# Optimization experiments

Hardware: AMD Instinct MI355X
Metric: run time of the kernel (lower is better)

The kernel has to match this reference:

```python
import jax, jax.numpy as jnp
import numpy as np

H = 32   # hidden_dim
L = 2    # rnn_num_layers
T = 52   # num_steps / seq_len
F = 64   # n_features (== 2*H, so layer-1 input size matches layer-0)
B = 8192 # batch


def _cell(x, h, c, Wih, Whh, b):
    # PyTorch LSTM gate order: i, f, g, o. b = b_ih + b_hh (mathematically identical).
    g = x @ Wih.T + h @ Whh.T + b
    i, f, gg, o = jnp.split(g, 4, axis=-1)
    c2 = jax.nn.sigmoid(f) * c + jax.nn.sigmoid(i) * jnp.tanh(gg)
    h2 = jax.nn.sigmoid(o) * jnp.tanh(c2)
    return h2, c2


def _encoder(x, h0, c0, Wih, Whh, b):
    # x: [B,T,F]; h0/c0: [2L,B,H]; PyTorch stacking order: [l0_fwd, l0_bwd, l1_fwd, l1_bwd]
    xs = jnp.swapaxes(x, 0, 1)  # time-major [T,B,F]
    hn, cn = [], []
    for l in range(L):
        def step_fwd(carry, xt):
            h, c = carry
            h2, c2 = _cell(xt, h, c, Wih[l, 0], Whh[l, 0], b[l, 0])
            return (h2, c2), h2
        def step_bwd(carry, xt):
            h, c = carry
            h2, c2 = _cell(xt, h, c, Wih[l, 1], Whh[l, 1], b[l, 1])
            return (h2, c2), h2
        (hf, cf), of = jax.lax.scan(step_fwd, (h0[2 * l], c0[2 * l]), xs)
        (hb, cb), ob = jax.lax.scan(step_bwd, (h0[2 * l + 1], c0[2 * l + 1]), xs[::-1])
        xs = jnp.concatenate([of, ob[::-1]], axis=-1)  # [T,B,2H]
        hn += [hf, hb]
        cn += [cf, cb]
    hn = jnp.stack(hn)  # [4,B,H]
    cn = jnp.stack(cn)
    hc = jnp.concatenate([jnp.swapaxes(hn, 0, 1), jnp.swapaxes(cn, 0, 1)], axis=1)  # [B,8,H]
    return hc.reshape(hc.shape[0], -1)  # [B, 2*2L*H] = [B,256]


def _decoder(code, Wih, Whh, b):
    Bn = code.shape[0]
    _code = code.reshape(Bn, 2, 2 * L, H)       # [B, (h,c), 4, H]
    h = jnp.swapaxes(_code[:, 0], 0, 1)          # [4,B,H]
    c = jnp.swapaxes(_code[:, 1], 0, 1)
    out0 = jnp.zeros((Bn, F), code.dtype)

    def step(carry, _):
        out, h, c = carry
        y = out
        hs, cs = [], []
        for l in range(L):
            hf, cf = _cell(y, h[2 * l], c[2 * l], Wih[l, 0], Whh[l, 0], b[l, 0])
            hb, cb = _cell(y, h[2 * l + 1], c[2 * l + 1], Wih[l, 1], Whh[l, 1], b[l, 1])
            y = jnp.concatenate([hf, hb], axis=-1)  # [B,2H]
            hs += [hf, hb]
            cs += [cf, cb]
        return (jax.lax.stop_gradient(y), jnp.stack(hs), jnp.stack(cs)), y

    _, ys = jax.lax.scan(step, (out0, h, c), None, length=T)  # ys: [T,B,F]
    return jnp.swapaxes(ys, 0, 1)  # [B,T,F]


def setup_inputs() -> dict:
    key = jax.random.key(0)
    ks = jax.random.split(key, 9)
    s = 1.0 / np.sqrt(H)  # PyTorch LSTM init range
    u = lambda k, shape: jax.random.uniform(k, shape, jnp.float32, -s, s)
    return {
        "x": jax.random.normal(ks[0], (B, T, F), jnp.float32),
        "h0": jax.random.normal(ks[1], (2 * L, B, H), jnp.float32),
        "c0": jax.random.normal(ks[2], (2 * L, B, H), jnp.float32),
        "enc_Wih": u(ks[3], (L, 2, 4 * H, F)),
        "enc_Whh": u(ks[4], (L, 2, 4 * H, H)),
        "enc_b": u(ks[5], (L, 2, 4 * H)),
        "dec_Wih": u(ks[6], (L, 2, 4 * H, F)),
        "dec_Whh": u(ks[7], (L, 2, 4 * H, H)),
        "dec_b": u(ks[8], (L, 2, 4 * H)),
    }


def reference(x, h0, c0, enc_Wih, enc_Whh, enc_b, dec_Wih, dec_Whh, dec_b):
    z = _encoder(x, h0, c0, enc_Wih, enc_Whh, enc_b)          # [B,256]
    x_hat = _decoder(z, dec_Wih, dec_Whh, dec_b)              # [B,T,F]
    return (x_hat, z)
```

## Files before the change

### kernel.cpp

```cpp
#include <hip/hip_runtime.h>
#include <cstddef>
#include <cstdint>

#define Tn 52
#define Fn 64
#define Hn 32
#define Bn 8192
#define XHAT_ELEMS (Bn * Tn * Fn)
#define L2E 1.44269504088896340736f

typedef __attribute__((ext_vector_type(8))) short bf8v;
typedef __attribute__((ext_vector_type(4))) float f4v;

__device__ __forceinline__ f4v mfma_bf16(bf8v a, bf8v b, f4v c) {
    return __builtin_amdgcn_mfma_f32_16x16x32_bf16(a, b, c, 0, 0, 0);
}

__device__ __forceinline__ unsigned short rne_bf16(float v) {
    unsigned b = __float_as_uint(v);
    unsigned r = ((b >> 16) & 1u) + 0x7FFFu;
    return (unsigned short)((b + r) >> 16);
}

__device__ __forceinline__ bf8v rne8(float4 a, float4 b) {
    float v[8] = {a.x, a.y, a.z, a.w, b.x, b.y, b.z, b.w};
    bf8v r;
#pragma unroll
    for (int j = 0; j < 8; ++j) r[j] = (short)rne_bf16(v[j]);
    return r;
}

__device__ __forceinline__ void lds_barrier() {
    __builtin_amdgcn_sched_barrier(0);
    asm volatile("s_waitcnt lgkmcnt(0)" ::: "memory");
    __builtin_amdgcn_s_barrier();
    __builtin_amdgcn_sched_barrier(0);
}

__device__ __forceinline__ float lstm_one(float aI, float aF, float aG, float aO, float& cst) {
    float ei = exp2f(fminf(40.f, -aI));
    float ef = exp2f(fminf(40.f, -aF));
    float eg = exp2f(fminf(40.f, -aG));
    float eo = exp2f(fminf(40.f, -aO));
    float p   = (1.f + ei) * (1.f + eg);
    float num = cst * p + (1.f - eg) * (1.f + ef);
    float den = (1.f + ef) * p;
    float c2  = num * __builtin_amdgcn_rcpf(den);
    cst = c2;
    float e2 = exp2f(fminf(40.f, -2.f * L2E * c2));
    return (1.f - e2) * __builtin_amdgcn_rcpf((1.f + eo) * (1.f + e2));
}

#define PINW(W)                                                               \
    asm volatile("" : "+v"(W[0][0]), "+v"(W[0][1]), "+v"(W[0][2]),            \
                      "+v"(W[1][0]), "+v"(W[1][1]), "+v"(W[1][2]));           \
    asm volatile("" : "+v"(W[2][0]), "+v"(W[2][1]), "+v"(W[2][2]),            \
                      "+v"(W[3][0]), "+v"(W[3][1]), "+v"(W[3][2]));

__global__ void prep_kernel(const float* __restrict__ eWih, const float* __restrict__ eWhh,
                            const float* __restrict__ dWih, const float* __restrict__ dWhh,
                            unsigned short* __restrict__ ws)
{
    int fid = blockIdx.x * 256 + threadIdx.x;
    if (fid >= 12288) return;
    int lane = fid & 63;
    int ki   = (fid >> 6) % 3;
    int nt   = (fid / 192) & 7;
    int cell = (fid / 1536) & 3;
    int grp  = fid / 6144;
    const float* Wih = grp ? dWih : eWih;
    const float* Whh = grp ? dWhh : eWhh;
    int gate = nt * 16 + (lane & 15);
    float scale = ((gate >> 5) == 2) ? 2.f * L2E : L2E;
    int k0 = ki * 32 + (lane >> 4) * 8;
    size_t base = (size_t)grp * 98304 + (size_t)cell * 12288 + nt * 1536 + ki * 512 + lane * 8;
#pragma unroll
    for (int j = 0; j < 8; ++j) {
        int k = k0 + j;
        float v = (k < 64) ? Wih[(size_t)cell * 8192 + gate * 64 + k]
                           : Whh[(size_t)cell * 4096 + gate * 32 + (k - 64)];
        ws[base + j] = rne_bf16(v * scale);
    }
}

template<int IS_L0>
__global__ __launch_bounds__(256, 2)
void enc_kernel(const float* __restrict__ X, const unsigned short* __restrict__ Xh,
                const float* __restrict__ h0, const float* __restrict__ c0,
                const unsigned short* __restrict__ Whi, const float* __restrict__ bias,
                int layer, unsigned short* __restrict__ outh, float* __restrict__ z)
{
    __shared__ __align__(16) unsigned short Hsh[2][2][16][40];
    const int tid = threadIdx.x, w = tid >> 6, lane = tid & 63;
    const int d = w >> 1, q = w & 1;
    const int a = lane & 15, kb = lane >> 4;
    const int u = q * 16 + a;
    const int row0 = blockIdx.x * 16;
    const int ci = 2 * layer + d;

    bf8v WH[4][3];
#pragma unroll
    for (int g = 0; g < 4; ++g)
#pragma unroll
        for (int ki = 0; ki < 3; ++ki)
            WH[g][ki] = *(const bf8v*)(Whi + (size_t)ci * 12288 + (2 * g + q) * 1536
                                       + ki * 512 + lane * 8);
    float bj[4];
#pragma unroll
    for (int g = 0; g < 4; ++g)
        bj[g] = bias[ci * 128 + g * 32 + u] * ((g == 2) ? 2.f * L2E : L2E);
    float cst[4], hfin[4];
#pragma unroll
    for (int j = 0; j < 4; ++j)
        cst[j] = c0[((size_t)ci * Bn + row0 + 4 * kb + j) * Hn + u];

    {
        int dd = tid >> 7, rr = (tid >> 3) & 15, u4 = (tid & 7) * 4;
        const float* src = h0 + ((size_t)(2 * layer + dd) * Bn + row0 + rr) * Hn + u4;
#pragma unroll
        for (int e = 0; e < 4; ++e)
            Hsh[dd][1][rr][u4 + e] = rne_bf16(src[e]);
    }
    __syncthreads();

    const int grow = row0 + a;
    float4 p0, p1, p2, p3; bf8v ph0, ph1;
    f4v acc[4];
    {
        int tt = d ? (Tn - 1) : 0;
        bf8v xf0, xf1;
        if (IS_L0) {
            const float* sp = X + ((size_t)grow * Tn + tt) * Fn;
            xf0 = rne8(*(const float4*)(sp + kb * 8), *(const float4*)(sp + kb * 8 + 4));
            xf1 = rne8(*(const float4*)(sp + 32 + kb * 8), *(const float4*)(sp + 32 + kb * 8 + 4));
        } else {
            size_t so = ((size_t)tt * Bn + grow) * Fn + kb * 8;
            xf0 = *(const bf8v*)(Xh + so);
            xf1 = *(const bf8v*)(Xh + so + 32);
        }
#pragma unroll
        for (int g = 0; g < 4; ++g) {
            acc[g] = (f4v){bj[g], bj[g], bj[g], bj[g]};
            acc[g] = mfma_bf16(xf0, WH[g][0], acc[g]);
            acc[g] = mfma_bf16(xf1, WH[g][1], acc[g]);
        }
        int tt1 = d ? (Tn - 2) : 1;
        if (IS_L0) {
            const float* sp = X + ((size_t)grow * Tn + tt1) * Fn;
            p0 = *(const float4*)(sp + kb * 8);      p1 = *(const float4*)(sp + kb * 8 + 4);
            p2 = *(const float4*)(sp + 32 + kb * 8); p3 = *(const float4*)(sp + 32 + kb * 8 + 4);
        } else {
            size_t so = ((size_t)tt1 * Bn + grow) * Fn + kb * 8;
            ph0 = *(const bf8v*)(Xh + so);
            ph1 = *(const bf8v*)(Xh + so + 32);
        }
    }

    for (int t = 0; t < Tn; ++t) {
        PINW(WH);
        bf8v hh = *(const bf8v*)&Hsh[d][(t & 1) ^ 1][a][kb * 8];
#pragma unroll
        for (int g = 0; g < 4; ++g) acc[g] = mfma_bf16(hh, WH[g][2], acc[g]);
        int tp = d ? (Tn - 1 - t) : t;
#pragma unroll
        for (int j = 0; j < 4; ++j) {
            float hv = lstm_one(acc[0][j], acc[1][j], acc[2][j], acc[3][j], cst[j]);
            hfin[j] = hv;
            unsigned short hp = rne_bf16(hv);
            Hsh[d][t & 1][4 * kb + j][u] = hp;
            if (IS_L0)
                outh[((size_t)tp * Bn + row0 + 4 * kb + j) * Fn + d * 32 + u] = hp;
        }
        {
            bf8v xf0, xf1;
            if (IS_L0) { xf0 = rne8(p0, p1); xf1 = rne8(p2, p3); }
            else       { xf0 = ph0; xf1 = ph1; }
#pragma unroll
            for (int g = 0; g < 4; ++g) {
                f4v t0 = (f4v){bj[g], bj[g], bj[g], bj[g]};
                t0 = mfma_bf16(xf0, WH[g][0], t0);
                acc[g] = mfma_bf16(xf1, WH[g][1], t0);
            }
            int ts = (t + 2 < Tn) ? t + 2 : Tn - 1;
            int tt = d ? (Tn - 1 - ts) : ts;
            if (IS_L0) {
                const float* sp = X + ((size_t)grow * Tn + tt) * Fn;
                p0 = *(const float4*)(sp + kb * 8);      p1 = *(const float4*)(sp + kb * 8 + 4);
                p2 = *(const float4*)(sp + 32 + kb * 8); p3 = *(const float4*)(sp + 32 + kb * 8 + 4);
            } else {
                size_t so = ((size_t)tt * Bn + grow) * Fn + kb * 8;
                ph0 = *(const bf8v*)(Xh + so);
                ph1 = *(const bf8v*)(Xh + so + 32);
            }
        }
        lds_barrier();
    }
#pragma unroll
    for (int j = 0; j < 4; ++j) {
        size_t zr = (size_t)(row0 + 4 * kb + j) * 256;
        z[zr + ci * 32 + u]       = hfin[j];
        z[zr + 128 + ci * 32 + u] = cst[j];
    }
}

__global__ __launch_bounds__(512, 2)
void dec_kernel(const unsigned short* __restrict__ Whi, const float* __restrict__ bias,
                const float* __restrict__ z, float* __restrict__ xhat)
{
    __shared__ __align__(16) unsigned short Ysh[2][2][16][72];
    __shared__ __align__(16) unsigned short Msh[2][16][72];
    __shared__ __align__(16) unsigned short Hsh[4][2][2][16][40];

    const int tid = threadIdx.x, w = tid >> 6, lane = tid & 63;
    const int P = w >> 2, cl = (w >> 1) & 1, q = w & 1;
    const int cell = P * 2 + cl;
    const int a = lane & 15, kb = lane >> 4, u = q * 16 + a;
    const int row0 = blockIdx.x * 32;

    bf8v WH[4][3];
#pragma unroll
    for (int g = 0; g < 4; ++g)
#pragma unroll
        for (int ki = 0; ki < 3; ++ki)
            WH[g][ki] = *(const bf8v*)(Whi + (size_t)cell * 12288 + (2 * g + q) * 1536
                                       + ki * 512 + lane * 8);
    float bj[4];
#pragma unroll
    for (int g = 0; g < 4; ++g)
        bj[g] = bias[cell * 128 + g * 32 + u] * ((g == 2) ? 2.f * L2E : L2E);

    float cst[2][4];
#pragma unroll
    for (int G = 0; G < 2; ++G)
#pragma unroll
        for (int j = 0; j < 4; ++j)
            cst[G][j] = z[(size_t)(row0 + G * 16 + 4 * kb + j) * 256 + 128 + cell * 32 + u];

    {
        int ct = tid >> 7, rem = tid & 127, rr = rem >> 2, u8 = (rem & 3) * 8;
        const float* src = z + (size_t)(row0 + rr) * 256 + ct * 32 + u8;
#pragma unroll
        for (int e = 0; e < 8; ++e)
            Hsh[ct][rr >> 4][1][rr & 15][u8 + e] = rne_bf16(src[e]);
    }
    __syncthreads();

    f4v accp[4];
    auto hpart = [&](int G, int rpar) {
        bf8v hh = *(const bf8v*)&Hsh[cell][G][rpar][a][kb * 8];
#pragma unroll
        for (int g = 0; g < 4; ++g) {
            f4v t0 = (f4v){bj[g], bj[g], bj[g], bj[g]};
            accp[g] = mfma_bf16(hh, WH[g][2], t0);
        }
    };
    auto finish = [&](int G, int t, bool isA, bool hasV) {
        if (hasV) {
            const unsigned short (*Vh)[72] = isA ? Ysh[G][(t - 1) & 1] : Msh[G];
            bf8v vh0 = *(const bf8v*)&Vh[a][kb * 8];
            bf8v vh1 = *(const bf8v*)&Vh[a][32 + kb * 8];
#pragma unroll
            for (int g = 0; g < 4; ++g) {
                accp[g] = mfma_bf16(vh0, WH[g][0], accp[g]);
                accp[g] = mfma_bf16(vh1, WH[g][1], accp[g]);
            }
        }
#pragma unroll
        for (int j = 0; j < 4; ++j) {
            float hv = lstm_one(accp[0][j], accp[1][j], accp[2][j], accp[3][j], cst[G][j]);
            unsigned short hp = rne_bf16(hv);
            int r = 4 * kb + j;
            Hsh[cell][G][t & 1][r][u] = hp;
            if (isA) {
                Msh[G][r][cl * 32 + u] = hp;
            } else {
                Ysh[G][t & 1][r][cl * 32 + u] = hp;
                xhat[((size_t)(row0 + G * 16 + r) * Tn + t) * Fn + cl * 32 + u] = hv;
            }
        }
    };

    hpart(0, 1);
    for (int t = 0; t < Tn; ++t) {
        PINW(WH);
        if (P == 0) { finish(0, t, true, t > 0);       hpart(1, (t - 1) & 1); }
        else        { if (t > 0) finish(1, t - 1, false, true); hpart(0, (t - 1) & 1); }
        lds_barrier();
        if (P == 0) { finish(1, t, true, t > 0);       hpart(0, t & 1); }
        else        { finish(0, t, false, true);       hpart(1, (t & 1) ^ 1); }
        lds_barrier();
    }
    if (P == 1) finish(1, Tn - 1, false, true);
}

extern "C" void kernel_launch(void* const* d_in, const int* in_sizes, int n_in,
                              void* d_out, int out_size, void* d_ws, size_t ws_size,
                              hipStream_t stream) {
    const float* x    = (const float*)d_in[0];
    const float* h0   = (const float*)d_in[1];
    const float* c0   = (const float*)d_in[2];
    const float* eWih = (const float*)d_in[3];
    const float* eWhh = (const float*)d_in[4];
    const float* eb   = (const float*)d_in[5];
    const float* dWih = (const float*)d_in[6];
    const float* dWhh = (const float*)d_in[7];
    const float* db   = (const float*)d_in[8];

    float* out = (float*)d_out;
    unsigned short* xs1h = (unsigned short*)d_out;
    float* zb = out + (size_t)XHAT_ELEMS;
    unsigned short* wsb = (unsigned short*)d_ws;

    hipLaunchKernelGGL(prep_kernel, dim3(48), dim3(256), 0, stream,
                       eWih, eWhh, dWih, dWhh, wsb);
    hipLaunchKernelGGL((enc_kernel<1>), dim3(Bn / 16), dim3(256), 0, stream,
                       x, (const unsigned short*)nullptr,
                       h0, c0, wsb, eb, 0, xs1h, zb);
    hipLaunchKernelGGL((enc_kernel<0>), dim3(Bn / 16), dim3(256), 0, stream,
                       (const float*)nullptr, xs1h,
                       h0, c0, wsb, eb, 1, (unsigned short*)nullptr, zb);
    hipLaunchKernelGGL(dec_kernel, dim3(Bn / 32), dim3(512), 0, stream,
                       wsb + 98304, db, zb, out);
}
```

Before: 267.6 us.

## Split encoder directions across blocks, unroll time loops, add MFMA priority

The encoder now launches one 128-thread block per direction (grid y = 2) instead of one 256-thread block holding both directions, which halves the barrier group size and shrinks shared memory per block. Both encoder and decoder time loops are unrolled by two so the double-buffer parity is a compile-time constant. Bias is pre-broadcast into vector registers and fed straight into the MFMA accumulator. The decoder MFMA sections are raised with s_setprio, and the sched_barrier fences around the LDS barrier are removed so the compiler can reorder across it. The risks are more, smaller blocks competing for CUs, and different instruction scheduling once the fences are gone.

After: 272.9 us. Within noise of the previous version (+2.0%).

```diff
diff --git a/kernel.cpp b/kernel.cpp
--- a/kernel.cpp
+++ b/kernel.cpp
@@ -31,10 +31,8 @@
 }
 
 __device__ __forceinline__ void lds_barrier() {
-    __builtin_amdgcn_sched_barrier(0);
     asm volatile("s_waitcnt lgkmcnt(0)" ::: "memory");
     __builtin_amdgcn_s_barrier();
-    __builtin_amdgcn_sched_barrier(0);
 }
 
 __device__ __forceinline__ float lstm_one(float aI, float aF, float aG, float aO, float& cst) {
@@ -84,18 +82,18 @@
 }
 
 template<int IS_L0>
-__global__ __launch_bounds__(256, 2)
+__global__ __launch_bounds__(128, 2)
 void enc_kernel(const float* __restrict__ X, const unsigned short* __restrict__ Xh,
                 const float* __restrict__ h0, const float* __restrict__ c0,
                 const unsigned short* __restrict__ Whi, const float* __restrict__ bias,
                 int layer, unsigned short* __restrict__ outh, float* __restrict__ z)
 {
-    __shared__ __align__(16) unsigned short Hsh[2][2][16][40];
-    const int tid = threadIdx.x, w = tid >> 6, lane = tid & 63;
-    const int d = w >> 1, q = w & 1;
+    __shared__ __align__(16) unsigned short Hsh[2][16][40];
+    const int tid = threadIdx.x, q = tid >> 6, lane = tid & 63;
     const int a = lane & 15, kb = lane >> 4;
     const int u = q * 16 + a;
     const int row0 = blockIdx.x * 16;
+    const int d = blockIdx.y;
     const int ci = 2 * layer + d;
 
     bf8v WH[4][3];
@@ -105,21 +103,23 @@
         for (int ki = 0; ki < 3; ++ki)
             WH[g][ki] = *(const bf8v*)(Whi + (size_t)ci * 12288 + (2 * g + q) * 1536
                                        + ki * 512 + lane * 8);
-    float bj[4];
-#pragma unroll
-    for (int g = 0; g < 4; ++g)
-        bj[g] = bias[ci * 128 + g * 32 + u] * ((g == 2) ? 2.f * L2E : L2E);
+    f4v bC[4];
+#pragma unroll
+    for (int g = 0; g < 4; ++g) {
+        float bv = bias[ci * 128 + g * 32 + u] * ((g == 2) ? 2.f * L2E : L2E);
+        bC[g] = (f4v){bv, bv, bv, bv};
+    }
     float cst[4], hfin[4];
 #pragma unroll
     for (int j = 0; j < 4; ++j)
         cst[j] = c0[((size_t)ci * Bn + row0 + 4 * kb + j) * Hn + u];
 
     {
-        int dd = tid >> 7, rr = (tid >> 3) & 15, u4 = (tid & 7) * 4;
-        const float* src = h0 + ((size_t)(2 * layer + dd) * Bn + row0 + rr) * Hn + u4;
+        int rr = tid >> 3, u4 = (tid & 7) * 4;
+        const float* src = h0 + ((size_t)ci * Bn + row0 + rr) * Hn + u4;
 #pragma unroll
         for (int e = 0; e < 4; ++e)
-            Hsh[dd][1][rr][u4 + e] = rne_bf16(src[e]);
+            Hsh[1][rr][u4 + e] = rne_bf16(src[e]);
     }
     __syncthreads();
 
@@ -139,11 +139,8 @@
             xf1 = *(const bf8v*)(Xh + so + 32);
         }
 #pragma unroll
-        for (int g = 0; g < 4; ++g) {
-            acc[g] = (f4v){bj[g], bj[g], bj[g], bj[g]};
-            acc[g] = mfma_bf16(xf0, WH[g][0], acc[g]);
-            acc[g] = mfma_bf16(xf1, WH[g][1], acc[g]);
-        }
+        for (int g = 0; g < 4; ++g)
+            acc[g] = mfma_bf16(xf1, WH[g][1], mfma_bf16(xf0, WH[g][0], bC[g]));
         int tt1 = d ? (Tn - 2) : 1;
         if (IS_L0) {
             const float* sp = X + ((size_t)grow * Tn + tt1) * Fn;
@@ -156,9 +153,9 @@
         }
     }
 
-    for (int t = 0; t < Tn; ++t) {
+    auto step = [&](int t, int par) {
         PINW(WH);
-        bf8v hh = *(const bf8v*)&Hsh[d][(t & 1) ^ 1][a][kb * 8];
+        bf8v hh = *(const bf8v*)&Hsh[par ^ 1][a][kb * 8];
 #pragma unroll
         for (int g = 0; g < 4; ++g) acc[g] = mfma_bf16(hh, WH[g][2], acc[g]);
         int tp = d ? (Tn - 1 - t) : t;
@@ -167,33 +164,32 @@
             float hv = lstm_one(acc[0][j], acc[1][j], acc[2][j], acc[3][j], cst[j]);
             hfin[j] = hv;
             unsigned short hp = rne_bf16(hv);
-            Hsh[d][t & 1][4 * kb + j][u] = hp;
+            Hsh[par][4 * kb + j][u] = hp;
             if (IS_L0)
                 outh[((size_t)tp * Bn + row0 + 4 * kb + j) * Fn + d * 32 + u] = hp;
         }
-        {
-            bf8v xf0, xf1;
-            if (IS_L0) { xf0 = rne8(p0, p1); xf1 = rne8(p2, p3); }
-            else       { xf0 = ph0; xf1 = ph1; }
-#pragma unroll
-            for (int g = 0; g < 4; ++g) {
-                f4v t0 = (f4v){bj[g], bj[g], bj[g], bj[g]};
-                t0 = mfma_bf16(xf0, WH[g][0], t0);
-                acc[g] = mfma_bf16(xf1, WH[g][1], t0);
-            }
-            int ts = (t + 2 < Tn) ? t + 2 : Tn - 1;
-            int tt = d ? (Tn - 1 - ts) : ts;
-            if (IS_L0) {
-                const float* sp = X + ((size_t)grow * Tn + tt) * Fn;
-                p0 = *(const float4*)(sp + kb * 8);      p1 = *(const float4*)(sp + kb * 8 + 4);
-                p2 = *(const float4*)(sp + 32 + kb * 8); p3 = *(const float4*)(sp + 32 + kb * 8 + 4);
-            } else {
-                size_t so = ((size_t)tt * Bn + grow) * Fn + kb * 8;
-                ph0 = *(const bf8v*)(Xh + so);
-                ph1 = *(const bf8v*)(Xh + so + 32);
-            }
-        }
-        lds_barrier();
+        bf8v xf0, xf1;
+        if (IS_L0) { xf0 = rne8(p0, p1); xf1 = rne8(p2, p3); }
+        else       { xf0 = ph0; xf1 = ph1; }
+#pragma unroll
+        for (int g = 0; g < 4; ++g)
+            acc[g] = mfma_bf16(xf1, WH[g][1], mfma_bf16(xf0, WH[g][0], bC[g]));
+        int ts = (t + 2 < Tn) ? t + 2 : Tn - 1;
+        int tt = d ? (Tn - 1 - ts) : ts;
+        if (IS_L0) {
+            const float* sp = X + ((size_t)grow * Tn + tt) * Fn;
+            p0 = *(const float4*)(sp + kb * 8);      p1 = *(const float4*)(sp + kb * 8 + 4);
+            p2 = *(const float4*)(sp + 32 + kb * 8); p3 = *(const float4*)(sp + 32 + kb * 8 + 4);
+        } else {
+            size_t so = ((size_t)tt * Bn + grow) * Fn + kb * 8;
+            ph0 = *(const bf8v*)(Xh + so);
+            ph1 = *(const bf8v*)(Xh + so + 32);
+        }
+        lds_barrier();
+    };
+    for (int it = 0; it < Tn / 2; ++it) {
+        step(2 * it, 0);
+        step(2 * it + 1, 1);
     }
 #pragma unroll
     for (int j = 0; j < 4; ++j) {
@@ -224,10 +220,12 @@
         for (int ki = 0; ki < 3; ++ki)
             WH[g][ki] = *(const bf8v*)(Whi + (size_t)cell * 12288 + (2 * g + q) * 1536
                                        + ki * 512 + lane * 8);
-    float bj[4];
-#pragma unroll
-    for (int g = 0; g < 4; ++g)
-        bj[g] = bias[cell * 128 + g * 32 + u] * ((g == 2) ? 2.f * L2E : L2E);
+    f4v bC[4];
+#pragma unroll
+    for (int g = 0; g < 4; ++g) {
+        float bv = bias[cell * 128 + g * 32 + u] * ((g == 2) ? 2.f * L2E : L2E);
+        bC[g] = (f4v){bv, bv, bv, bv};
+    }
 
     float cst[2][4];
 #pragma unroll
@@ -248,49 +246,59 @@
     f4v accp[4];
     auto hpart = [&](int G, int rpar) {
         bf8v hh = *(const bf8v*)&Hsh[cell][G][rpar][a][kb * 8];
-#pragma unroll
-        for (int g = 0; g < 4; ++g) {
-            f4v t0 = (f4v){bj[g], bj[g], bj[g], bj[g]};
-            accp[g] = mfma_bf16(hh, WH[g][2], t0);
-        }
+        __builtin_amdgcn_s_setprio(1);
+#pragma unroll
+        for (int g = 0; g < 4; ++g) accp[g] = mfma_bf16(hh, WH[g][2], bC[g]);
+        __builtin_amdgcn_s_setprio(0);
     };
-    auto finish = [&](int G, int t, bool isA, bool hasV) {
+    auto finish = [&](int G, int t, int par, bool isA, bool hasV) {
         if (hasV) {
-            const unsigned short (*Vh)[72] = isA ? Ysh[G][(t - 1) & 1] : Msh[G];
+            const unsigned short (*Vh)[72] = isA ? Ysh[G][par ^ 1] : Msh[G];
             bf8v vh0 = *(const bf8v*)&Vh[a][kb * 8];
             bf8v vh1 = *(const bf8v*)&Vh[a][32 + kb * 8];
+            __builtin_amdgcn_s_setprio(1);
 #pragma unroll
             for (int g = 0; g < 4; ++g) {
                 accp[g] = mfma_bf16(vh0, WH[g][0], accp[g]);
                 accp[g] = mfma_bf16(vh1, WH[g][1], accp[g]);
             }
+            __builtin_amdgcn_s_setprio(0);
         }
 #pragma unroll
         for (int j = 0; j < 4; ++j) {
             float hv = lstm_one(accp[0][j], accp[1][j], accp[2][j], accp[3][j], cst[G][j]);
             unsigned short hp = rne_bf16(hv);
             int r = 4 * kb + j;
-            Hsh[cell][G][t & 1][r][u] = hp;
+            Hsh[cell][G][par][r][u] = hp;
             if (isA) {
                 Msh[G][r][cl * 32 + u] = hp;
             } else {
-                Ysh[G][t & 1][r][cl * 32 + u] = hp;
+                Ysh[G][par][r][cl * 32 + u] = hp;
                 xhat[((size_t)(row0 + G * 16 + r) * Tn + t) * Fn + cl * 32 + u] = hv;
             }
         }
     };
 
     hpart(0, 1);
-    for (int t = 0; t < Tn; ++t) {
+    for (int it = 0; it < Tn / 2; ++it) {
+        const int t0 = 2 * it, t1 = t0 + 1;
+        const bool nz = (it > 0);
         PINW(WH);
-        if (P == 0) { finish(0, t, true, t > 0);       hpart(1, (t - 1) & 1); }
-        else        { if (t > 0) finish(1, t - 1, false, true); hpart(0, (t - 1) & 1); }
-        lds_barrier();
-        if (P == 0) { finish(1, t, true, t > 0);       hpart(0, t & 1); }
-        else        { finish(0, t, false, true);       hpart(1, (t & 1) ^ 1); }
-        lds_barrier();
-    }
-    if (P == 1) finish(1, Tn - 1, false, true);
+        if (P == 0) { finish(0, t0, 0, true, nz);            hpart(1, 1); }
+        else        { if (nz) finish(1, t0 - 1, 1, false, true); hpart(0, 1); }
+        lds_barrier();
+        if (P == 0) { finish(1, t0, 0, true, nz);            hpart(0, 0); }
+        else        { finish(0, t0, 0, false, true);         hpart(1, 1); }
+        lds_barrier();
+        PINW(WH);
+        if (P == 0) { finish(0, t1, 1, true, true);          hpart(1, 0); }
+        else        { finish(1, t0, 0, false, true);         hpart(0, 0); }
+        lds_barrier();
+        if (P == 0) { finish(1, t1, 1, true, true);          hpart(0, 1); }
+        else        { finish(0, t1, 1, false, true);         hpart(1, 0); }
+        lds_barrier();
+    }
+    if (P == 1) finish(1, Tn - 1, 1, false, true);
 }
 
 extern "C" void kernel_launch(void* const* d_in, const int* in_sizes, int n_in,
@@ -313,10 +321,10 @@
 
     hipLaunchKernelGGL(prep_kernel, dim3(48), dim3(256), 0, stream,
                        eWih, eWhh, dWih, dWhh, wsb);
-    hipLaunchKernelGGL((enc_kernel<1>), dim3(Bn / 16), dim3(256), 0, stream,
+    hipLaunchKernelGGL((enc_kernel<1>), dim3(Bn / 16, 2), dim3(128), 0, stream,
                        x, (const unsigned short*)nullptr,
                        h0, c0, wsb, eb, 0, xs1h, zb);
-    hipLaunchKernelGGL((enc_kernel<0>), dim3(Bn / 16), dim3(256), 0, stream,
+    hipLaunchKernelGGL((enc_kernel<0>), dim3(Bn / 16, 2), dim3(128), 0, stream,
                        (const float*)nullptr, xs1h,
                        h0, c0, wsb, eb, 1, (unsigned short*)nullptr, zb);
     hipLaunchKernelGGL(dec_kernel, dim3(Bn / 32), dim3(512), 0, stream,
```
